# Kernel tuning notes

Measured on AMD Instinct MI355X. Metric: run time of the kernel, lower is better.

The kernel has to match this reference:

```python
import jax, jax.numpy as jnp
import numpy as np

EPS = 1e-12


def setup_inputs() -> dict:
    key = jax.random.key(0)
    k1, k2, k3 = jax.random.split(key, 3)
    N, D, K = 131072, 64, 1024
    input_data = jax.random.normal(k1, (N, D), dtype=jnp.float32)
    codebooks = jax.random.normal(k2, (K, D), dtype=jnp.float32)
    random_vector = jax.random.normal(k3, (N, D), dtype=jnp.float32)
    return {"input_data": input_data, "codebooks": codebooks, "random_vector": random_vector}


def reference(input_data, codebooks, random_vector):
    # input_data: (N, D); codebooks: (K, D); random_vector: (N, D)
    N = input_data.shape[0]
    K = codebooks.shape[0]

    distances = (
        jnp.sum(input_data ** 2, axis=1, keepdims=True)
        - 2.0 * (input_data @ codebooks.T)
        + jnp.sum(codebooks ** 2, axis=1)[None, :]
    )
    min_indices = jnp.argmin(distances, axis=1)  # (N,)
    hard_quantized_input = codebooks[min_indices]  # (N, D) gather

    # Noise-substitution VQ: replace residual with a random vector of equal norm
    norm_residual = jnp.sqrt(jnp.sum((input_data - hard_quantized_input) ** 2, axis=1, keepdims=True))
    norm_random = jnp.sqrt(jnp.sum(random_vector ** 2, axis=1, keepdims=True))
    vq_error = (norm_residual / (norm_random + EPS)) * random_vector
    quantized_input = input_data + vq_error

    # Usage counts via scatter-add (equivalent to one-hot encodings mean)
    counts = jnp.zeros((K,), dtype=jnp.int32).at[min_indices].add(1)
    avg_probs = counts.astype(jnp.float32) / jnp.float32(N)
    perplexity = jnp.exp(-jnp.sum(avg_probs * jnp.log(avg_probs + EPS)))

    codebooks_used = counts  # torch module accumulates; fresh buffer starts at zero
    return quantized_input, perplexity, codebooks_used
```

## Files before the change

### kernel.cpp

```cpp
#include <hip/hip_runtime.h>
#include <math.h>


#define NSVQ_D 64
#define ABN 512

typedef __attribute__((ext_vector_type(8))) _Float16 half8;
typedef __attribute__((ext_vector_type(16))) float f32x16;

__global__ __launch_bounds__(256)
void nsvq_prep(const float* __restrict__ cb,
               ushort* __restrict__ cbf,
               float* __restrict__ cn2k, int* __restrict__ counts, int K) {
  if (blockIdx.x == 0) ((int4*)counts)[threadIdx.x] = make_int4(0, 0, 0, 0);
  int r = blockIdx.x * 256 + threadIdx.x;
  if (r >= K) return;
  const float* row = cb + (long)r * NSVQ_D;
  float nrm = 0.f;
#pragma unroll
  for (int j = 0; j < 8; ++j) {
    float4 v0 = *(const float4*)(row + j * 8);
    float4 v1 = *(const float4*)(row + j * 8 + 4);
    float f[8] = {v0.x, v0.y, v0.z, v0.w, v1.x, v1.y, v1.z, v1.w};
    half8 hv;
#pragma unroll
    for (int e = 0; e < 8; ++e) {
      nrm = fmaf(f[e], f[e], nrm);
      hv[e] = (_Float16)f[e];
    }
    int blk = (r >> 5) * 256 + (j >> 1) * 64 + (j & 1) * 32 + (r & 31);
    *(half8*)(cbf + blk * 8) = hv;
  }
  cn2k[r] = 2048.f * (nrm + 512.f);
}

__global__ __launch_bounds__(1024, 1)
void nsvq_fused(const float* __restrict__ x,
                const ushort* __restrict__ cbf,
                const float* __restrict__ cn2k,
                const float* __restrict__ rv,
                int* __restrict__ counts,
                float* __restrict__ out) {
  __shared__ ushort CS[65536];
  __shared__ float CN[1024];
  __shared__ uint bestLds[ABN];
  __shared__ int hist[1024];

  const int tid = threadIdx.x;
  const int lane = tid & 63;
  const int wid = tid >> 6;
  const int l31 = lane & 31;
  const int lh = lane >> 5;
  const long brow = (long)blockIdx.x * ABN;
  const int wrow = wid * 32;

#pragma unroll
  for (int i = 0; i < 8; ++i) {
    int e = i * 1024 + tid;
    ((uint4*)CS)[e] = ((const uint4*)cbf)[e];
  }
  CN[tid] = cn2k[tid];
  hist[tid] = 0;

  half8 ax[4];
  float4 xf[8];
  float xxloc = 0.f;
  const long grow = brow + wrow + l31;
#pragma unroll
  for (int ks = 0; ks < 4; ++ks) {
    const float* xr = x + grow * NSVQ_D + ks * 16 + lh * 8;
    float4 v0 = *(const float4*)xr;
    float4 v1 = *(const float4*)(xr + 4);
    xf[ks * 2] = v0;
    xf[ks * 2 + 1] = v1;
    xxloc += v0.x * v0.x + v0.y * v0.y + v0.z * v0.z + v0.w * v0.w;
    xxloc += v1.x * v1.x + v1.y * v1.y + v1.z * v1.z + v1.w * v1.w;
    half8 h;
    h[0] = (_Float16)(v0.x * -4096.f); h[1] = (_Float16)(v0.y * -4096.f);
    h[2] = (_Float16)(v0.z * -4096.f); h[3] = (_Float16)(v0.w * -4096.f);
    h[4] = (_Float16)(v1.x * -4096.f); h[5] = (_Float16)(v1.y * -4096.f);
    h[6] = (_Float16)(v1.z * -4096.f); h[7] = (_Float16)(v1.w * -4096.f);
    ax[ks] = h;
  }

  uint u1[16];
#pragma unroll
  for (int i = 0; i < 16; ++i) u1[i] = 0xFFFFFFFFu;

  __syncthreads();

  auto LOADL = [&](half8 (&B)[4], float& cn, int g) {
    const ushort* p = CS + (g * 256 + lane) * 8;
#pragma unroll
    for (int ks = 0; ks < 4; ++ks) B[ks] = *(const half8*)(p + ks * 512);
    cn = CN[g * 32 + l31];
  };
  auto COMPUTE = [&](const half8 (&B)[4], float cc, int g) {
    const uint kidx = (uint)(g * 32 + l31);
    f32x16 a = {cc, cc, cc, cc, cc, cc, cc, cc, cc, cc, cc, cc, cc, cc, cc, cc};
    a = __builtin_amdgcn_mfma_f32_32x32x16_f16(ax[0], B[0], a, 0, 0, 0);
    a = __builtin_amdgcn_mfma_f32_32x32x16_f16(ax[1], B[1], a, 0, 0, 0);
    a = __builtin_amdgcn_mfma_f32_32x32x16_f16(ax[2], B[2], a, 0, 0, 0);
    a = __builtin_amdgcn_mfma_f32_32x32x16_f16(ax[3], B[3], a, 0, 0, 0);
#pragma unroll
    for (int r = 0; r < 16; ++r) {
      uint m = (__float_as_uint(a[r]) & 0xFFFFFC00u) | kidx;
      u1[r] = min(u1[r], m);
    }
  };

  half8 BA[4], BB[4];
  float cnA, cnB;
  LOADL(BA, cnA, 0);
  LOADL(BB, cnB, 1);

  for (int g = 0; g < 32; g += 2) {
    COMPUTE(BA, cnA, g);
    LOADL(BA, cnA, (g + 2) & 31);
    COMPUTE(BB, cnB, g + 1);
    LOADL(BB, cnB, (g + 3) & 31);
  }

#pragma unroll
  for (int r = 0; r < 16; ++r) {
    uint a1 = u1[r];
#pragma unroll
    for (int off = 1; off < 32; off <<= 1)
      a1 = min(a1, (uint)__shfl_xor((int)a1, off));
    if (l31 == 0) {
      int rowloc = (r & 3) + 8 * (r >> 2) + 4 * lh;
      bestLds[wrow + rowloc] = a1;
    }
  }

  uint p = bestLds[wrow + l31];
  uint k = p & 1023u;
  float sraw = __uint_as_float(p & 0xFFFFFC00u);

  float4 rr[8];
  float drnd = 0.f;
#pragma unroll
  for (int ks = 0; ks < 4; ++ks) {
    const float* rp = rv + grow * NSVQ_D + ks * 16 + lh * 8;
    float4 r0 = *(const float4*)rp;
    float4 r1 = *(const float4*)(rp + 4);
    rr[ks * 2] = r0;
    rr[ks * 2 + 1] = r1;
    drnd += r0.x * r0.x + r0.y * r0.y + r0.z * r0.z + r0.w * r0.w;
    drnd += r1.x * r1.x + r1.y * r1.y + r1.z * r1.z + r1.w * r1.w;
  }
  float xx = xxloc + __shfl_xor(xxloc, 32, 64);
  drnd += __shfl_xor(drnd, 32, 64);
  float dres = fmaxf(fmaf(sraw, 1.f / 2048.f, xx - 512.f), 0.f);
  float scale = sqrtf(dres) / (sqrtf(drnd) + 1e-12f);

#pragma unroll
  for (int ks = 0; ks < 4; ++ks) {
    float* op = out + grow * NSVQ_D + ks * 16 + lh * 8;
    float4 x0 = xf[ks * 2], x1 = xf[ks * 2 + 1];
    float4 r0 = rr[ks * 2], r1 = rr[ks * 2 + 1];
    float4 o0, o1;
    o0.x = x0.x + scale * r0.x; o0.y = x0.y + scale * r0.y;
    o0.z = x0.z + scale * r0.z; o0.w = x0.w + scale * r0.w;
    o1.x = x1.x + scale * r1.x; o1.y = x1.y + scale * r1.y;
    o1.z = x1.z + scale * r1.z; o1.w = x1.w + scale * r1.w;
    *(float4*)op = o0;
    *(float4*)(op + 4) = o1;
  }
  if (lh == 0) atomicAdd(&hist[k], 1);

  __syncthreads();
  int v = hist[tid];
  if (v) atomicAdd(&counts[tid], v);
}

__global__ void nsvq_perp_kernel(const int* __restrict__ counts,
                                 float* __restrict__ out_tail,
                                 float invN, int K) {
  int t = threadIdx.x;
  float v = 0.f;
  if (t < K) {
    int c = counts[t];
    out_tail[1 + t] = (float)c;
    float p = (float)c * invN;
    v = p * logf(p + 1e-12f);
  }
#pragma unroll
  for (int off = 1; off < 64; off <<= 1) v += __shfl_xor(v, off, 64);
  __shared__ float red[16];
  int wid = t >> 6;
  if ((t & 63) == 0) red[wid] = v;
  __syncthreads();
  if (t == 0) {
    float s = 0.f;
    int nw = (blockDim.x + 63) / 64;
    for (int w = 0; w < nw; ++w) s += red[w];
    out_tail[0] = expf(-s);
  }
}

extern "C" void kernel_launch(void* const* d_in, const int* in_sizes, int n_in,
                              void* d_out, int out_size, void* d_ws, size_t ws_size,
                              hipStream_t stream) {
  const float* x  = (const float*)d_in[0];
  const float* cb = (const float*)d_in[1];
  const float* rv = (const float*)d_in[2];
  float* out = (float*)d_out;

  const int D = NSVQ_D;
  const int N = in_sizes[0] / D;
  const int K = in_sizes[1] / D;

  float*  cn2k   = (float*)d_ws;
  int*    counts = (int*)((char*)d_ws + 4096);
  ushort* cbf    = (ushort*)((char*)d_ws + 8192);

  nsvq_prep<<<(K + 255) / 256, 256, 0, stream>>>(cb, cbf, cn2k, counts, K);
  nsvq_fused<<<N / ABN, 1024, 0, stream>>>(x, cbf, cn2k, rv, counts, out);
  nsvq_perp_kernel<<<1, 1024, 0, stream>>>(counts, out + (size_t)N * D, 1.0f / (float)N, K);
}
```

Baseline: 49.25 us.

## Drop LDS codebook staging and read fp16 codebook directly from global/L2

Removes the 128KB shared-memory copy of the fp16 codebook and its norms, so each wave streams codebook fragments straight from global memory (expected to stay in L2). Blocks shrink to 256 threads and 128 rows, with launch bounds allowing two blocks per CU. This removes the per-block staging cost and the single-block-per-CU limit that the large LDS footprint imposed. In exchange every wave re-reads the whole codebook through the cache hierarchy, with higher latency than LDS, and there are four times as many blocks each doing histogram flush atomics.

Result: slower. 57.28 us (+16.3%).

```diff
diff --git a/kernel.cpp b/kernel.cpp
--- a/kernel.cpp
+++ b/kernel.cpp
@@ -3,7 +3,7 @@
 
 
 #define NSVQ_D 64
-#define ABN 512
+#define ABN 128
 
 typedef __attribute__((ext_vector_type(8))) _Float16 half8;
 typedef __attribute__((ext_vector_type(16))) float f32x16;
@@ -34,17 +34,16 @@
   cn2k[r] = 2048.f * (nrm + 512.f);
 }
 
-__global__ __launch_bounds__(1024, 1)
+__global__ __launch_bounds__(256, 2)
 void nsvq_fused(const float* __restrict__ x,
                 const ushort* __restrict__ cbf,
                 const float* __restrict__ cn2k,
                 const float* __restrict__ rv,
                 int* __restrict__ counts,
                 float* __restrict__ out) {
-  __shared__ ushort CS[65536];
-  __shared__ float CN[1024];
   __shared__ uint bestLds[ABN];
   __shared__ int hist[1024];
+  ((int4*)hist)[threadIdx.x] = make_int4(0, 0, 0, 0);
 
   const int tid = threadIdx.x;
   const int lane = tid & 63;
@@ -53,14 +52,6 @@
   const int lh = lane >> 5;
   const long brow = (long)blockIdx.x * ABN;
   const int wrow = wid * 32;
-
-#pragma unroll
-  for (int i = 0; i < 8; ++i) {
-    int e = i * 1024 + tid;
-    ((uint4*)CS)[e] = ((const uint4*)cbf)[e];
-  }
-  CN[tid] = cn2k[tid];
-  hist[tid] = 0;
 
   half8 ax[4];
   float4 xf[8];
@@ -89,11 +80,11 @@
 
   __syncthreads();
 
-  auto LOADL = [&](half8 (&B)[4], float& cn, int g) {
-    const ushort* p = CS + (g * 256 + lane) * 8;
+  auto LOAD = [&](half8 (&B)[4], float& cn, int g) {
+    const ushort* p = cbf + g * 2048 + lane * 8;
 #pragma unroll
     for (int ks = 0; ks < 4; ++ks) B[ks] = *(const half8*)(p + ks * 512);
-    cn = CN[g * 32 + l31];
+    cn = cn2k[g * 32 + l31];
   };
   auto COMPUTE = [&](const half8 (&B)[4], float cc, int g) {
     const uint kidx = (uint)(g * 32 + l31);
@@ -111,14 +102,14 @@
 
   half8 BA[4], BB[4];
   float cnA, cnB;
-  LOADL(BA, cnA, 0);
-  LOADL(BB, cnB, 1);
+  LOAD(BA, cnA, 0);
+  LOAD(BB, cnB, 1);
 
   for (int g = 0; g < 32; g += 2) {
     COMPUTE(BA, cnA, g);
-    LOADL(BA, cnA, (g + 2) & 31);
+    LOAD(BA, cnA, (g + 2) & 31);
     COMPUTE(BB, cnB, g + 1);
-    LOADL(BB, cnB, (g + 3) & 31);
+    LOAD(BB, cnB, (g + 3) & 31);
   }
 
 #pragma unroll
@@ -170,8 +161,14 @@
   if (lh == 0) atomicAdd(&hist[k], 1);
 
   __syncthreads();
-  int v = hist[tid];
-  if (v) atomicAdd(&counts[tid], v);
+  int v0 = hist[tid];
+  int v1 = hist[tid + 256];
+  int v2 = hist[tid + 512];
+  int v3 = hist[tid + 768];
+  if (v0) atomicAdd(&counts[tid], v0);
+  if (v1) atomicAdd(&counts[tid + 256], v1);
+  if (v2) atomicAdd(&counts[tid + 512], v2);
+  if (v3) atomicAdd(&counts[tid + 768], v3);
 }
 
 __global__ void nsvq_perp_kernel(const int* __restrict__ counts,
@@ -216,6 +213,6 @@
   ushort* cbf    = (ushort*)((char*)d_ws + 8192);
 
   nsvq_prep<<<(K + 255) / 256, 256, 0, stream>>>(cb, cbf, cn2k, counts, K);
-  nsvq_fused<<<N / ABN, 1024, 0, stream>>>(x, cbf, cn2k, rv, counts, out);
+  nsvq_fused<<<N / ABN, 256, 0, stream>>>(x, cbf, cn2k, rv, counts, out);
   nsvq_perp_kernel<<<1, 1024, 0, stream>>>(counts, out + (size_t)N * D, 1.0f / (float)N, K);
 }
```
